# Kernel optimization log

Hardware: AMD Instinct MI355X
Metric: run time of the kernel (lower is better)

The kernel has to match this reference:

```python
import jax, jax.numpy as jnp
import numpy as np

K = 4
EPS = 1e-5
NEG_SLOPE = 0.2


def _edge_feature(coor_q, x_q, coor_k, x_k, k):
    """coor_*: [B,3,G*], x_q: [B,C,Gq], x_k: [B,C,Gk] -> [B,2C,Gq,k]"""
    B = x_k.shape[0]
    cq = jax.lax.stop_gradient(coor_q)
    ck = jax.lax.stop_gradient(coor_k)
    # squared pairwise distances [B, Gq, Gk]
    q2 = jnp.sum(cq * cq, axis=1)  # [B,Gq]
    k2 = jnp.sum(ck * ck, axis=1)  # [B,Gk]
    dist = q2[:, :, None] + k2[:, None, :] - 2.0 * jnp.einsum('bcq,bck->bqk', cq, ck)
    _, idx = jax.lax.top_k(-dist, k)  # k nearest, idx: [B,Gq,k]
    xk_t = jnp.transpose(x_k, (0, 2, 1))  # [B,Gk,C]
    feat = xk_t[jnp.arange(B)[:, None, None], idx]  # [B,Gq,k,C] gather
    feat = jnp.transpose(feat, (0, 3, 1, 2))  # [B,C,Gq,k]
    xq = jnp.broadcast_to(x_q[:, :, :, None], feat.shape)
    return jnp.concatenate([feat - xq, xq], axis=1)


def _group_norm(x, gamma, beta, groups):
    # x: [B,C,G,k], normalize per (group, sample) over (C//groups, G, k)
    B, C, G, k = x.shape
    xr = x.reshape(B, groups, -1)
    mean = jnp.mean(xr, axis=-1, keepdims=True)
    var = jnp.var(xr, axis=-1, keepdims=True)
    xn = ((xr - mean) * jax.lax.rsqrt(var + EPS)).reshape(B, C, G, k)
    return xn * gamma[None, :, None, None] + beta[None, :, None, None]


def _block(x, W, gamma, beta):
    # 1x1 conv (no bias) + GroupNorm(4) + LeakyReLU(0.2)
    y = jnp.einsum('oc,bcgk->bogk', W, x)
    y = _group_norm(y, gamma, beta, 4)
    return jax.nn.leaky_relu(y, NEG_SLOPE)


def setup_inputs() -> dict:
    key = jax.random.key(0)
    ks = jax.random.split(key, 10)
    B, C, Gs, Gd = 16, 384, 4096, 1024
    return {
        'coor': jax.random.normal(ks[0], (B, 3, Gs), jnp.float32),
        'f': jax.random.normal(ks[1], (B, C, Gs), jnp.float32),
        'coor_q': jax.random.normal(ks[2], (B, 3, Gd), jnp.float32),
        'f_q': jax.random.normal(ks[3], (B, C, Gd), jnp.float32),
        'W1': jax.random.normal(ks[4], (512, 2 * C), jnp.float32) * 0.02,
        'g1': jnp.ones((512,), jnp.float32),
        'b1': jnp.zeros((512,), jnp.float32),
        'W2': jax.random.normal(ks[5], (C, 1024), jnp.float32) * 0.02,
        'g2': jnp.ones((C,), jnp.float32),
        'b2': jnp.zeros((C,), jnp.float32),
    }


def reference(coor, f, coor_q, f_q, W1, g1, b1, W2, g2, b2):
    e1 = _edge_feature(coor_q, f_q, coor, f, K)        # [B,768,Gd,k]
    h = jnp.max(_block(e1, W1, g1, b1), axis=-1)       # [B,512,Gd]
    e2 = _edge_feature(coor_q, h, coor_q, h, K)        # [B,1024,Gd,k]
    out = jnp.max(_block(e2, W2, g2, b2), axis=-1)     # [B,384,Gd]
    return out
```

## Files before the change

### kernel.cpp

```cpp
#include <hip/hip_runtime.h>
#include <stdint.h>

#define B_   16
#define CIN  384
#define GS   4096
#define GD   1024
#define M1   512
#define K2C  512
#define M2   384
#define ROWS2 768
#define NEG  0.2f
#define EPS_ 1e-5f

typedef __bf16 bf16x8 __attribute__((ext_vector_type(8)));
typedef float  f32x4  __attribute__((ext_vector_type(4)));
typedef float  f32x2  __attribute__((ext_vector_type(2)));
typedef unsigned long long u64k;

__device__ __forceinline__ float bf2f(ushort u) {
  uint32_t v = ((uint32_t)u) << 16;
  return __builtin_bit_cast(float, v);
}
__device__ __forceinline__ ushort f2bf(float f) {
  uint32_t x = __builtin_bit_cast(uint32_t, f);
  x += 0x7FFFu + ((x >> 16) & 1u);
  return (ushort)(x >> 16);
}

__device__ __forceinline__ f32x2 pk_mul(f32x2 a, f32x2 b) {
  f32x2 d; asm("v_pk_mul_f32 %0, %1, %2" : "=v"(d) : "v"(a), "v"(b)); return d;
}
__device__ __forceinline__ f32x2 pk_add(f32x2 a, f32x2 b) {
  f32x2 d; asm("v_pk_add_f32 %0, %1, %2" : "=v"(d) : "v"(a), "v"(b)); return d;
}
__device__ __forceinline__ f32x2 pk_fma(f32x2 a, f32x2 b, f32x2 c) {
  f32x2 d; asm("v_pk_fma_f32 %0, %1, %2, %3" : "=v"(d) : "v"(a), "v"(b), "v"(c)); return d;
}

__device__ __forceinline__ void gload16(const void* g, void* l) {
  __builtin_amdgcn_global_load_lds(
      (const __attribute__((address_space(1))) void*)g,
      (__attribute__((address_space(3))) void*)l, 16, 0, 0);
}

__global__ void k_prep(const float* __restrict__ W1, const float* __restrict__ W2,
                       ushort* __restrict__ W1a, ushort* __restrict__ W1d,
                       ushort* __restrict__ W2a, ushort* __restrict__ W2d,
                       const float* __restrict__ cs, const float* __restrict__ cqv,
                       float* __restrict__ s2s, float* __restrict__ s2q) {
#pragma clang fp contract(off)
  int blk = blockIdx.x;
  if (blk < 768) {
    int t = blk * 256 + threadIdx.x;
    int o = t / 384, c = t % 384;
    float wa = W1[(size_t)o * 768 + c];
    float wb = W1[(size_t)o * 768 + 384 + c];
    W1a[t] = f2bf(wa);
    W1d[t] = f2bf(wb - wa);
  } else if (blk < 1536) {
    int t = (blk - 768) * 256 + threadIdx.x;
    int o = t / 512, c = t % 512;
    float wa = W2[(size_t)o * 1024 + c];
    float wb = W2[(size_t)o * 1024 + 512 + c];
    W2a[t] = f2bf(wa);
    W2d[t] = f2bf(wb - wa);
  } else {
    int u = blk - 1536;
    int b = u / 20;
    int i = (u % 20) * 256 + threadIdx.x;
    if (i < GS) {
      const float* cb = cs + (size_t)b * 3 * GS;
      float x = cb[i], y = cb[GS + i], z = cb[2 * GS + i];
      s2s[(size_t)b * GS + i] = (x * x + y * y) + z * z;
    } else {
      int j = i - GS;
      const float* cb = cqv + (size_t)b * 3 * GD;
      float x = cb[j], y = cb[GD + j], z = cb[2 * GD + j];
      s2q[(size_t)b * GD + j] = (x * x + y * y) + z * z;
    }
  }
}

__device__ __forceinline__ uint32_t dmap(float d) {
  uint32_t u = __builtin_bit_cast(uint32_t, d);
  return u ^ (((uint32_t)((int32_t)u >> 31)) | 0x80000000u);
}
__device__ __forceinline__ u64k mkkey(uint32_t hi, uint32_t lo) {
  uint2 t; t.x = lo; t.y = hi;
  return __builtin_bit_cast(u64k, t);
}
__device__ __forceinline__ void kce(u64k& a, u64k& b) {
  bool c = b < a;
  u64k lo = c ? b : a, hi = c ? a : b;
  a = lo; b = hi;
}
__device__ __forceinline__ void klmin(u64k& a, u64k b) { a = b < a ? b : a; }

template<int GSRC>
__global__ __launch_bounds__(256) void k_knn(const float* __restrict__ cq,
                                             const float* __restrict__ ck,
                                             const float* __restrict__ s2qry,
                                             const float* __restrict__ s2src,
                                             int* __restrict__ idx) {
  constexpr int ITERS = GSRC / 256;
  static_assert(ITERS % 2 == 0, "even iteration count required for 2-deep unroll");
  int tid = threadIdx.x;
  int lane = tid & 63, wv = tid >> 6;
  int b = blockIdx.y;
  int qA = blockIdx.x * 8 + wv * 2;
  int qB = qA + 1;
  const float* cqb = cq + (size_t)b * 3 * GD;
  const float* ckb = ck + (size_t)b * 3 * GSRC;
  const float* s2b = s2src + (size_t)b * GSRC;
  float qxA = cqb[qA], qyA = cqb[GD + qA], qzA = cqb[2 * GD + qA];
  float qxB = cqb[qB], qyB = cqb[GD + qB], qzB = cqb[2 * GD + qB];
  float q2A = s2qry[(size_t)b * GD + qA];
  float q2B = s2qry[(size_t)b * GD + qB];
  f32x2 qxpA = {qxA, qxA}, qypA = {qyA, qyA}, qzpA = {qzA, qzA}, q2pA = {q2A, q2A};
  f32x2 qxpB = {qxB, qxB}, qypB = {qyB, qyB}, qzpB = {qzB, qzB}, q2pB = {q2B, q2B};
  f32x2 m2p = {-2.f, -2.f};

  u64k kA0 = ~0ull, kA1 = ~0ull, kA2 = ~0ull, kA3 = ~0ull;
  u64k kB0 = ~0ull, kB1 = ~0ull, kB2 = ~0ull, kB3 = ~0ull;

#define KNN_Q(QXP, QYP, QZP, Q2P, K0, K1, K2, K3)                              \
  {                                                                            \
    f32x2 dotl = pk_add(pk_add(pk_mul(QXP, xl), pk_mul(QYP, yl)), pk_mul(QZP, zl)); \
    f32x2 doth = pk_add(pk_add(pk_mul(QXP, xh), pk_mul(QYP, yh)), pk_mul(QZP, zh)); \
    f32x2 dl = pk_fma(dotl, m2p, pk_add(Q2P, sl));                             \
    f32x2 dh = pk_fma(doth, m2p, pk_add(Q2P, sh));                             \
    u64k n0 = mkkey(dmap(dl.x), j0u);                                          \
    u64k n1 = mkkey(dmap(dl.y), j0u + 1);                                      \
    u64k n2 = mkkey(dmap(dh.x), j0u + 2);                                      \
    u64k n3 = mkkey(dmap(dh.y), j0u + 3);                                      \
    kce(n0, n1); kce(n2, n3); kce(n0, n2); kce(n1, n3); kce(n1, n2);           \
    klmin(K0, n3); klmin(K1, n2); klmin(K2, n1); klmin(K3, n0);                \
    kce(K0, K2); kce(K1, K3); kce(K0, K1); kce(K2, K3);                        \
  }

#define KNN_STEP(Xv, Yv, Zv, Sv, J0)                                           \
  {                                                                            \
    f32x2 xl = {Xv.x, Xv.y}, xh = {Xv.z, Xv.w};                                \
    f32x2 yl = {Yv.x, Yv.y}, yh = {Yv.z, Yv.w};                                \
    f32x2 zl = {Zv.x, Zv.y}, zh = {Zv.z, Zv.w};                                \
    f32x2 sl = {Sv.x, Sv.y}, sh = {Sv.z, Sv.w};                                \
    uint32_t j0u = (uint32_t)(J0);                                             \
    KNN_Q(qxpA, qypA, qzpA, q2pA, kA0, kA1, kA2, kA3);                         \
    KNN_Q(qxpB, qypB, qzpB, q2pB, kB0, kB1, kB2, kB3);                         \
  }

#define KNN_LOAD(Xv, Yv, Zv, Sv, J)                                            \
  {                                                                            \
    Xv = *reinterpret_cast<const float4*>(ckb + (J));                          \
    Yv = *reinterpret_cast<const float4*>(ckb + GSRC + (J));                   \
    Zv = *reinterpret_cast<const float4*>(ckb + 2 * GSRC + (J));               \
    Sv = *reinterpret_cast<const float4*>(s2b + (J));                          \
  }

  int base = lane * 4;
  float4 X0, Y0, Z0, S0, X1, Y1, Z1, S1;
  KNN_LOAD(X0, Y0, Z0, S0, base);
  for (int it = 0; it < ITERS; it += 2) {
    int j0 = it * 256 + base;
    KNN_LOAD(X1, Y1, Z1, S1, j0 + 256);
    KNN_STEP(X0, Y0, Z0, S0, j0);
    if (it + 2 < ITERS) KNN_LOAD(X0, Y0, Z0, S0, j0 + 512);
    KNN_STEP(X1, Y1, Z1, S1, j0 + 256);
  }
#undef KNN_STEP
#undef KNN_Q
#undef KNN_LOAD

#pragma unroll
  for (int off = 1; off < 64; off <<= 1) {
    u64k p0 = __shfl_xor(kA0, off), p1 = __shfl_xor(kA1, off);
    u64k p2 = __shfl_xor(kA2, off), p3 = __shfl_xor(kA3, off);
    klmin(kA0, p3); klmin(kA1, p2); klmin(kA2, p1); klmin(kA3, p0);
    kce(kA0, kA2); kce(kA1, kA3); kce(kA0, kA1); kce(kA2, kA3);
    u64k r0 = __shfl_xor(kB0, off), r1 = __shfl_xor(kB1, off);
    u64k r2 = __shfl_xor(kB2, off), r3 = __shfl_xor(kB3, off);
    klmin(kB0, r3); klmin(kB1, r2); klmin(kB2, r1); klmin(kB3, r0);
    kce(kB0, kB2); kce(kB1, kB3); kce(kB0, kB1); kce(kB2, kB3);
  }
  if (lane == 0) {
    int4 ra;
    ra.x = (int)(uint32_t)kA0; ra.y = (int)(uint32_t)kA1;
    ra.z = (int)(uint32_t)kA2; ra.w = (int)(uint32_t)kA3;
    *reinterpret_cast<int4*>(&idx[((size_t)b * GD + qA) * 4]) = ra;
    int4 rb;
    rb.x = (int)(uint32_t)kB0; rb.y = (int)(uint32_t)kB1;
    rb.z = (int)(uint32_t)kB2; rb.w = (int)(uint32_t)kB3;
    *reinterpret_cast<int4*>(&idx[((size_t)b * GD + qB) * 4]) = rb;
  }
}

template<bool OUT_BF16>
__global__ __launch_bounds__(256) void k_gemmF(const ushort* __restrict__ W,
                                               const float* __restrict__ X32,
                                               void* __restrict__ outv,
                                               int M, int Kd, int N) {
  __shared__ __align__(16) ushort As[128 * 32];
  __shared__ __align__(16) ushort Bs[128 * 40];
  int b = blockIdx.z;
  const float* X = X32 + (size_t)b * Kd * N;
  int m0 = blockIdx.y * 128, n0 = blockIdx.x * 128;
  int tid = threadIdx.x;
  int w = tid >> 6, lane = tid & 63;
  int lr = lane & 15, lq = lane >> 4;
  int mw = (w >> 1) * 64, nw = (w & 1) * 64;
  int r0 = tid >> 2, c0 = tid & 3;

  ushort* dA0 = As + w * 512;
  ushort* dA1 = As + 2048 + w * 512;
  const ushort* gA0 = W + (size_t)(m0 + r0) * Kd + c0 * 8;
  const ushort* gA1 = W + (size_t)(m0 + r0 + 64) * Kd + c0 * 8;

  int bn = tid & 127;
  int bm = tid >> 7;

  f32x4 zero = {0.f, 0.f, 0.f, 0.f};
  f32x4 acc[4][4];
#pragma unroll
  for (int mi = 0; mi < 4; mi++)
#pragma unroll
    for (int ni = 0; ni < 4; ni++) acc[mi][ni] = zero;

  int nk = Kd / 32;
  for (int kt = 0; kt < nk; kt++) {
    int kk = kt * 32;
    __syncthreads();
    gload16(gA0 + kk, dA0);
    gload16(gA1 + kk, dA1);
#pragma unroll
    for (int pp = 0; pp < 8; pp++) {
      int m = pp * 2 + bm;
      int k = kk + 2 * m;
      float va = X[(size_t)k * N + n0 + bn];
      float vb = X[(size_t)(k + 1) * N + n0 + bn];
      ushort2 pkv; pkv.x = f2bf(va); pkv.y = f2bf(vb);
      *reinterpret_cast<ushort2*>(&Bs[bn * 40 + 2 * m]) = pkv;
    }
    __syncthreads();
    bf16x8 af[4], bfr[4];
#pragma unroll
    for (int mi = 0; mi < 4; mi++)
      af[mi] = *reinterpret_cast<const bf16x8*>(&As[(mw + mi * 16 + lr) * 32 + lq * 8]);
#pragma unroll
    for (int ni = 0; ni < 4; ni++)
      bfr[ni] = *reinterpret_cast<const bf16x8*>(&Bs[(nw + ni * 16 + lr) * 40 + lq * 8]);
#pragma unroll
    for (int mi = 0; mi < 4; mi++)
#pragma unroll
      for (int ni = 0; ni < 4; ni++)
        acc[mi][ni] = __builtin_amdgcn_mfma_f32_16x16x32_bf16(af[mi], bfr[ni], acc[mi][ni], 0, 0, 0);
  }
#pragma unroll
  for (int mi = 0; mi < 4; mi++) {
    int m = m0 + mw + mi * 16 + lq * 4;
#pragma unroll
    for (int ni = 0; ni < 4; ni++) {
      int n = n0 + nw + ni * 16 + lr;
#pragma unroll
      for (int r = 0; r < 4; r++) {
        size_t off = (size_t)b * M * N + (size_t)(m + r) * N + n;
        if constexpr (OUT_BF16) ((ushort*)outv)[off] = f2bf(acc[mi][ni][r]);
        else                    ((float*)outv)[off] = acc[mi][ni][r];
      }
    }
  }
}

template<bool OUT_BF16>
__global__ __launch_bounds__(256) void k_gemm(const ushort* __restrict__ W,
                                              const ushort* __restrict__ Xt,
                                              void* __restrict__ outv,
                                              int M, int Kd, int N) {
  __shared__ __align__(16) ushort As[128 * 32];
  __shared__ __align__(16) ushort Bs[128 * 32];
  int b = blockIdx.z;
  const ushort* X = Xt + (size_t)b * N * Kd;
  int m0 = blockIdx.y * 128, n0 = blockIdx.x * 128;
  int tid = threadIdx.x;
  int w = tid >> 6, lane = tid & 63;
  int lr = lane & 15, lq = lane >> 4;
  int mw = (w >> 1) * 64, nw = (w & 1) * 64;
  int r0 = tid >> 2, c0 = tid & 3;

  ushort* dA0 = As + w * 512;
  ushort* dA1 = As + 2048 + w * 512;
  ushort* dB0 = Bs + w * 512;
  ushort* dB1 = Bs + 2048 + w * 512;
  const ushort* gA0 = W + (size_t)(m0 + r0) * Kd + c0 * 8;
  const ushort* gA1 = W + (size_t)(m0 + r0 + 64) * Kd + c0 * 8;
  const ushort* gB0 = X + (size_t)(n0 + r0) * Kd + c0 * 8;
  const ushort* gB1 = X + (size_t)(n0 + r0 + 64) * Kd + c0 * 8;

  f32x4 zero = {0.f, 0.f, 0.f, 0.f};
  f32x4 acc[4][4];
#pragma unroll
  for (int mi = 0; mi < 4; mi++)
#pragma unroll
    for (int ni = 0; ni < 4; ni++) acc[mi][ni] = zero;

  int nk = Kd / 32;
  for (int kt = 0; kt < nk; kt++) {
    int kk = kt * 32;
    __syncthreads();
    gload16(gA0 + kk, dA0);
    gload16(gA1 + kk, dA1);
    gload16(gB0 + kk, dB0);
    gload16(gB1 + kk, dB1);
    __syncthreads();
    bf16x8 af[4], bfr[4];
#pragma unroll
    for (int mi = 0; mi < 4; mi++)
      af[mi] = *reinterpret_cast<const bf16x8*>(&As[(mw + mi * 16 + lr) * 32 + lq * 8]);
#pragma unroll
    for (int ni = 0; ni < 4; ni++)
      bfr[ni] = *reinterpret_cast<const bf16x8*>(&Bs[(nw + ni * 16 + lr) * 32 + lq * 8]);
#pragma unroll
    for (int mi = 0; mi < 4; mi++)
#pragma unroll
      for (int ni = 0; ni < 4; ni++)
        acc[mi][ni] = __builtin_amdgcn_mfma_f32_16x16x32_bf16(af[mi], bfr[ni], acc[mi][ni], 0, 0, 0);
  }
#pragma unroll
  for (int mi = 0; mi < 4; mi++) {
    int m = m0 + mw + mi * 16 + lq * 4;
#pragma unroll
    for (int ni = 0; ni < 4; ni++) {
      int n = n0 + nw + ni * 16 + lr;
#pragma unroll
      for (int r = 0; r < 4; r++) {
        size_t off = (size_t)b * M * N + (size_t)(m + r) * N + n;
        if constexpr (OUT_BF16) ((ushort*)outv)[off] = f2bf(acc[mi][ni][r]);
        else                    ((float*)outv)[off] = acc[mi][ni][r];
      }
    }
  }
}

__global__ __launch_bounds__(256) void k_stats1y(const ushort* __restrict__ A,
                                                 const float* __restrict__ Bq,
                                                 const int* __restrict__ idx1,
                                                 const float* __restrict__ gam,
                                                 float* __restrict__ Ysel,
                                                 float* __restrict__ part) {
  __shared__ __align__(16) ushort Arow[GS];
  __shared__ __align__(16) int ids[GD * 4];
  __shared__ float rs[256], rq[256];
  int s = blockIdx.x, grp = blockIdx.y, b = blockIdx.z;
  int tid = threadIdx.x;
  for (int i = tid; i < GD; i += 256) {
    int4 v = *reinterpret_cast<const int4*>(&idx1[((size_t)b * GD + i) * 4]);
    v.x &= (GS - 1); v.y &= (GS - 1); v.z &= (GS - 1); v.w &= (GS - 1);
    *reinterpret_cast<int4*>(&ids[i * 4]) = v;
  }
  float sum = 0.f, ssq = 0.f;
  for (int oi = 0; oi < 16; oi++) {
    int o = grp * 128 + s * 16 + oi;
    const ushort* Ar = A + ((size_t)b * M1 + o) * GS;
    __syncthreads();
#pragma unroll
    for (int i = tid * 8; i < GS; i += 2048)
      *reinterpret_cast<uint4*>(&Arow[i]) = *reinterpret_cast<const uint4*>(&Ar[i]);
    __syncthreads();
    const float* Br = Bq + ((size_t)b * M1 + o) * GD;
    float* Yr = Ysel + ((size_t)b * M1 + o) * GD;
    float sgn = gam[o];
    for (int g = tid; g < GD; g += 256) {
      int4 id = *reinterpret_cast<const int4*>(&ids[g * 4]);
      float base = Br[g];
      float y0 = bf2f(Arow[id.x]) + base;
      float y1 = bf2f(Arow[id.y]) + base;
      float y2 = bf2f(Arow[id.z]) + base;
      float y3 = bf2f(Arow[id.w]) + base;
      sum += y0 + y1 + y2 + y3;
      ssq += y0 * y0 + y1 * y1 + y2 * y2 + y3 * y3;
      float mx = fmaxf(fmaxf(y0, y1), fmaxf(y2, y3));
      float mn = fminf(fminf(y0, y1), fminf(y2, y3));
      Yr[g] = (sgn >= 0.f) ? mx : mn;
    }
  }
  rs[tid] = sum; rq[tid] = ssq;
  __syncthreads();
  for (int t = 128; t > 0; t >>= 1) {
    if (tid < t) { rs[tid] += rs[tid + t]; rq[tid] += rq[tid + t]; }
    __syncthreads();
  }
  if (tid == 0) {
    int key = ((b * 4 + grp) * 8 + s) * 2;
    part[key] = rs[0]; part[key + 1] = rq[0];
  }
}

__global__ __launch_bounds__(256) void k_stats2y(const float* __restrict__ Y2,
                                                 const int* __restrict__ idx2,
                                                 const float* __restrict__ gam,
                                                 float* __restrict__ Ysel,
                                                 float* __restrict__ part) {
  __shared__ __align__(16) float Arow[GD];
  __shared__ __align__(16) int ids[GD * 4];
  __shared__ float rs[256], rq[256];
  int s = blockIdx.x, grp = blockIdx.y, b = blockIdx.z;
  int tid = threadIdx.x;
  for (int i = tid; i < GD; i += 256) {
    int4 v = *reinterpret_cast<const int4*>(&idx2[((size_t)b * GD + i) * 4]);
    v.x &= (GD - 1); v.y &= (GD - 1); v.z &= (GD - 1); v.w &= (GD - 1);
    *reinterpret_cast<int4*>(&ids[i * 4]) = v;
  }
  float sum = 0.f, ssq = 0.f;
  for (int oi = 0; oi < 12; oi++) {
    int o = grp * 96 + s * 12 + oi;
    const float* Ar = Y2 + ((size_t)b * ROWS2 + o) * GD;
    __syncthreads();
#pragma unroll
    for (int i = tid * 4; i < GD; i += 1024)
      *reinterpret_cast<float4*>(&Arow[i]) = *reinterpret_cast<const float4*>(&Ar[i]);
    __syncthreads();
    const float* Br = Y2 + ((size_t)b * ROWS2 + 384 + o) * GD;
    float* Yr = Ysel + ((size_t)b * M2 + o) * GD;
    float sgn = gam[o];
    for (int g = tid; g < GD; g += 256) {
      int4 id = *reinterpret_cast<const int4*>(&ids[g * 4]);
      float base = Br[g];
      float y0 = Arow[id.x] + base;
      float y1 = Arow[id.y] + base;
      float y2 = Arow[id.z] + base;
      float y3 = Arow[id.w] + base;
      sum += y0 + y1 + y2 + y3;
      ssq += y0 * y0 + y1 * y1 + y2 * y2 + y3 * y3;
      float mx = fmaxf(fmaxf(y0, y1), fmaxf(y2, y3));
      float mn = fminf(fminf(y0, y1), fminf(y2, y3));
      Yr[g] = (sgn >= 0.f) ? mx : mn;
    }
  }
  rs[tid] = sum; rq[tid] = ssq;
  __syncthreads();
  for (int t = 128; t > 0; t >>= 1) {
    if (tid < t) { rs[tid] += rs[tid + t]; rq[tid] += rq[tid + t]; }
    __syncthreads();
  }
  if (tid == 0) {
    int key = ((b * 4 + grp) * 8 + s) * 2;
    part[key] = rs[0]; part[key + 1] = rq[0];
  }
}

__global__ void k_h2(const float* __restrict__ Ysel, const float* __restrict__ part,
                     const float* __restrict__ gam, const float* __restrict__ bet,
                     ushort* __restrict__ hT) {
  __shared__ ushort tile[64][66];
  int g0 = blockIdx.x * 64, o0 = blockIdx.y * 64, b = blockIdx.z;
  int tid = threadIdx.x;
  int tkey = b * 4 + (o0 >> 7);
  float s = 0.f, q = 0.f;
#pragma unroll
  for (int i = 0; i < 8; i++) { s += part[(tkey * 8 + i) * 2]; q += part[(tkey * 8 + i) * 2 + 1]; }
  float mean = s * (1.0f / 524288.0f);
  float var = q * (1.0f / 524288.0f) - mean * mean;
  float rstd = 1.0f / sqrtf(fmaxf(var, 0.0f) + EPS_);
  int gx = tid & 63, oy = tid >> 6;
#pragma unroll
  for (int oi = 0; oi < 16; oi++) {
    int ol = oi * 4 + oy;
    int o = o0 + ol;
    float y = Ysel[((size_t)b * M1 + o) * GD + g0 + gx];
    float v = (y - mean) * rstd * gam[o] + bet[o];
    v = v >= 0.f ? v : NEG * v;
    tile[ol][gx] = f2bf(v);
  }
  __syncthreads();
  int col = tid & 63, r4 = tid >> 6;
#pragma unroll
  for (int i = 0; i < 16; i++) {
    int gl = i * 4 + r4;
    hT[((size_t)b * GD + g0 + gl) * K2C + o0 + col] = tile[col][gl];
  }
}

__global__ void k_out2(const float* __restrict__ Ysel2, const float* __restrict__ part,
                       const float* __restrict__ gam, const float* __restrict__ bet,
                       float* __restrict__ out) {
  int b = blockIdx.z, o = blockIdx.y;
  int g = blockIdx.x * 256 + threadIdx.x;
  int tkey = b * 4 + o / 96;
  float s = 0.f, q = 0.f;
#pragma unroll
  for (int i = 0; i < 8; i++) { s += part[(tkey * 8 + i) * 2]; q += part[(tkey * 8 + i) * 2 + 1]; }
  float mean = s * (1.0f / 393216.0f);
  float var = q * (1.0f / 393216.0f) - mean * mean;
  float rstd = 1.0f / sqrtf(fmaxf(var, 0.0f) + EPS_);
  float y = Ysel2[((size_t)b * M2 + o) * GD + g];
  float v = (y - mean) * rstd * gam[o] + bet[o];
  v = v >= 0.f ? v : NEG * v;
  out[((size_t)b * M2 + o) * GD + g] = v;
}

extern "C" void kernel_launch(void* const* d_in, const int* in_sizes, int n_in,
                              void* d_out, int out_size, void* d_ws, size_t ws_size,
                              hipStream_t stream) {
  (void)in_sizes; (void)n_in; (void)out_size;
  const float* coor  = (const float*)d_in[0];
  const float* f     = (const float*)d_in[1];
  const float* coorq = (const float*)d_in[2];
  const float* fq    = (const float*)d_in[3];
  const float* W1    = (const float*)d_in[4];
  const float* g1    = (const float*)d_in[5];
  const float* b1    = (const float*)d_in[6];
  const float* W2    = (const float*)d_in[7];
  const float* g2    = (const float*)d_in[8];
  const float* b2    = (const float*)d_in[9];

  if (ws_size < 182468608u) return;

  char* ws = (char*)d_ws;
  int*    idx1 = (int*)(ws + 0);
  int*    idx2 = (int*)(ws + 0x40000);
  float*  s1p  = (float*)(ws + 0x80000);
  float*  s2p  = (float*)(ws + 0x82000);
  ushort* W1a  = (ushort*)(ws + 0x84000);
  ushort* W1d  = W1a + (size_t)512 * 384;
  ushort* W2a  = W1d + (size_t)512 * 384;
  ushort* W2d  = W2a + (size_t)384 * 512;
  ushort* fT   = W2d + (size_t)384 * 512;
  ushort* fqT  = fT + (size_t)B_ * GS * CIN;
  ushort* Abuf = fqT + (size_t)B_ * GD * CIN;
  float*  Bq   = (float*)(Abuf + (size_t)B_ * M1 * GS);
  ushort* hT   = (ushort*)((char*)Bq + (size_t)B_ * M1 * GD * 4);
  float*  Y2   = (float*)fT;
  float*  Ysel1 = (float*)fT;
  float*  Ysel2 = (float*)Abuf;
  float*  s2s  = (float*)hT;
  float*  s2q  = s2s + (size_t)B_ * GS;

  k_prep<<<dim3(1856), 256, 0, stream>>>(W1, W2, W1a, W1d, W2a, W2d,
                                         coor, coorq, s2s, s2q);

  k_knn<GS><<<dim3(GD / 8, B_), 256, 0, stream>>>(coorq, coor, s2q, s2s, idx1);
  k_knn<GD><<<dim3(GD / 8, B_), 256, 0, stream>>>(coorq, coorq, s2q, s2q, idx2);

  k_gemmF<true ><<<dim3(GS / 128, M1 / 128, B_), 256, 0, stream>>>(W1a, f, Abuf, M1, CIN, GS);
  k_gemmF<false><<<dim3(GD / 128, M1 / 128, B_), 256, 0, stream>>>(W1d, fq, Bq, M1, CIN, GD);

  k_stats1y<<<dim3(8, 4, B_), 256, 0, stream>>>(Abuf, Bq, idx1, g1, Ysel1, s1p);
  k_h2<<<dim3(GD / 64, M1 / 64, B_), 256, 0, stream>>>(Ysel1, s1p, g1, b1, hT);

  k_gemm<false><<<dim3(GD / 128, ROWS2 / 128, B_), 256, 0, stream>>>(W2a, hT, Y2, ROWS2, K2C, GD);

  k_stats2y<<<dim3(8, 4, B_), 256, 0, stream>>>(Y2, idx2, g2, Ysel2, s2p);
  k_out2<<<dim3(GD / 256, M2, B_), 256, 0, stream>>>(Ysel2, s2p, g2, b2, (float*)d_out);
}
```

Before: 438.1 us.

## Prefetch fp32 B tile into registers and repack LDS layout for 16-byte stores

The fp32-input GEMM now loads the next K-slice of X into registers while the current slice's MFMAs run, so global load latency overlaps with compute instead of sitting between barriers. The B tile's shared-memory layout becomes [k-group][n][8], so each thread converts 8 values and writes them with one 16-byte store instead of eight 4-byte stores. Fragment reads now index this new layout. It costs 16 extra registers per thread, which may lower occupancy.

```diff
diff --git a/kernel.cpp b/kernel.cpp
--- a/kernel.cpp
+++ b/kernel.cpp
@@ -200,7 +200,7 @@
                                                void* __restrict__ outv,
                                                int M, int Kd, int N) {
   __shared__ __align__(16) ushort As[128 * 32];
-  __shared__ __align__(16) ushort Bs[128 * 40];
+  __shared__ __align__(16) ushort Bs[4 * 128 * 8];
   int b = blockIdx.z;
   const float* X = X32 + (size_t)b * Kd * N;
   int m0 = blockIdx.y * 128, n0 = blockIdx.x * 128;
@@ -216,7 +216,32 @@
   const ushort* gA1 = W + (size_t)(m0 + r0 + 64) * Kd + c0 * 8;
 
   int bn = tid & 127;
-  int bm = tid >> 7;
+  int bg = tid >> 7;
+  const float* Xcol = X + n0 + bn;
+
+  float pb[16];
+
+#define LOADB(KK)                                                              \
+  {                                                                            \
+    _Pragma("unroll")                                                          \
+    for (int gg = 0; gg < 2; gg++) {                                           \
+      const float* Xg = Xcol + (size_t)((KK) + (bg + gg * 2) * 8) * N;         \
+      _Pragma("unroll")                                                        \
+      for (int j = 0; j < 8; j++) pb[gg * 8 + j] = Xg[(size_t)j * N];          \
+    }                                                                          \
+  }
+#define STOREB()                                                               \
+  {                                                                            \
+    _Pragma("unroll")                                                          \
+    for (int gg = 0; gg < 2; gg++) {                                           \
+      uint4 pkv;                                                               \
+      pkv.x = (uint32_t)f2bf(pb[gg * 8 + 0]) | ((uint32_t)f2bf(pb[gg * 8 + 1]) << 16); \
+      pkv.y = (uint32_t)f2bf(pb[gg * 8 + 2]) | ((uint32_t)f2bf(pb[gg * 8 + 3]) << 16); \
+      pkv.z = (uint32_t)f2bf(pb[gg * 8 + 4]) | ((uint32_t)f2bf(pb[gg * 8 + 5]) << 16); \
+      pkv.w = (uint32_t)f2bf(pb[gg * 8 + 6]) | ((uint32_t)f2bf(pb[gg * 8 + 7]) << 16); \
+      *reinterpret_cast<uint4*>(&Bs[((bg + gg * 2) * 128 + bn) * 8]) = pkv;    \
+    }                                                                          \
+  }
 
   f32x4 zero = {0.f, 0.f, 0.f, 0.f};
   f32x4 acc[4][4];
@@ -226,34 +251,30 @@
     for (int ni = 0; ni < 4; ni++) acc[mi][ni] = zero;
 
   int nk = Kd / 32;
+  LOADB(0);
   for (int kt = 0; kt < nk; kt++) {
     int kk = kt * 32;
     __syncthreads();
     gload16(gA0 + kk, dA0);
     gload16(gA1 + kk, dA1);
-#pragma unroll
-    for (int pp = 0; pp < 8; pp++) {
-      int m = pp * 2 + bm;
-      int k = kk + 2 * m;
-      float va = X[(size_t)k * N + n0 + bn];
-      float vb = X[(size_t)(k + 1) * N + n0 + bn];
-      ushort2 pkv; pkv.x = f2bf(va); pkv.y = f2bf(vb);
-      *reinterpret_cast<ushort2*>(&Bs[bn * 40 + 2 * m]) = pkv;
-    }
-    __syncthreads();
+    STOREB();
+    __syncthreads();
+    if (kt + 1 < nk) LOADB(kk + 32);
     bf16x8 af[4], bfr[4];
 #pragma unroll
     for (int mi = 0; mi < 4; mi++)
       af[mi] = *reinterpret_cast<const bf16x8*>(&As[(mw + mi * 16 + lr) * 32 + lq * 8]);
 #pragma unroll
     for (int ni = 0; ni < 4; ni++)
-      bfr[ni] = *reinterpret_cast<const bf16x8*>(&Bs[(nw + ni * 16 + lr) * 40 + lq * 8]);
+      bfr[ni] = *reinterpret_cast<const bf16x8*>(&Bs[(lq * 128 + nw + ni * 16 + lr) * 8]);
 #pragma unroll
     for (int mi = 0; mi < 4; mi++)
 #pragma unroll
       for (int ni = 0; ni < 4; ni++)
         acc[mi][ni] = __builtin_amdgcn_mfma_f32_16x16x32_bf16(af[mi], bfr[ni], acc[mi][ni], 0, 0, 0);
   }
+#undef LOADB
+#undef STOREB
 #pragma unroll
   for (int mi = 0; mi < 4; mi++) {
     int m = m0 + mw + mi * 16 + lq * 4;
```

Result: no change. 430.5 us (-1.7%).
